# Kernel tuning notes

Measured on AMD Instinct MI355X. Metric: run time of the kernel, lower is better.

## Reference

```python
import math
import jax, jax.numpy as jnp
import numpy as np

B, S, DIM = 1, 2048, 2880
N_HEADS, N_KV, HD = 64, 8, 64
ROPE_FACTOR = 32.0
THETA = 150000.0
NEG_INF = -1e30


def setup_inputs() -> dict:
    key = jax.random.key(0)
    ks = jax.random.split(key, 12)
    std = 0.02
    x = jax.random.normal(ks[0], (B, S, DIM), jnp.float32)
    # rope cache: (S, 2*HD) = [cos | sin], rotate_half convention (angles duplicated)
    inv_freq = 1.0 / (THETA ** (np.arange(0, HD, 2, dtype=np.float32) / HD))
    angles = np.arange(S, dtype=np.float32)[:, None] * inv_freq[None, :]   # (S, HD/2)
    emb = np.concatenate([angles, angles], axis=-1)                        # (S, HD)
    rope_cache = jnp.asarray(np.concatenate([np.cos(emb), np.sin(emb)], axis=-1))  # (S, 2*HD)
    wq_w = jax.random.normal(ks[1], (N_HEADS * HD, DIM), jnp.float32) * std
    wq_b = jax.random.normal(ks[2], (N_HEADS * HD,), jnp.float32) * std
    wk_w = jax.random.normal(ks[3], (N_KV * HD, DIM), jnp.float32) * std
    wk_b = jax.random.normal(ks[4], (N_KV * HD,), jnp.float32) * std
    wv_w = jax.random.normal(ks[5], (N_KV * HD, DIM), jnp.float32) * std
    wv_b = jax.random.normal(ks[6], (N_KV * HD,), jnp.float32) * std
    wo_w = jax.random.normal(ks[7], (DIM, N_HEADS * HD), jnp.float32) * std
    wo_b = jax.random.normal(ks[8], (DIM,), jnp.float32) * std
    sinks = jax.random.normal(ks[9], (N_HEADS,), jnp.float32) * std
    return {"x": x, "rope_cache": rope_cache, "wq_w": wq_w, "wq_b": wq_b,
            "wk_w": wk_w, "wk_b": wk_b, "wv_w": wv_w, "wv_b": wv_b,
            "wo_w": wo_w, "wo_b": wo_b, "sinks": sinks, "sliding_window": 128}


def _rotate_half(t):
    t1, t2 = t[..., : HD // 2], t[..., HD // 2 :]
    return jnp.concatenate([-t2, t1], axis=-1)


def reference(x, rope_cache, wq_w, wq_b, wk_w, wk_b, wv_w, wv_b, wo_w, wo_b, sinks, sliding_window):
    bsz, seqlen, _ = x.shape
    mscale = 0.1 * math.log(ROPE_FACTOR) + 1.0
    scale = mscale / math.sqrt(HD)

    q = (x @ wq_w.T + wq_b).reshape(bsz, seqlen, N_HEADS, HD)
    k = (x @ wk_w.T + wk_b).reshape(bsz, seqlen, N_KV, HD)
    v = (x @ wv_w.T + wv_b).reshape(bsz, seqlen, N_KV, HD)

    cos = rope_cache[:seqlen, :HD][None, :, None, :]   # (1,S,1,HD)
    sin = rope_cache[:seqlen, HD:][None, :, None, :]
    q = q * cos + _rotate_half(q) * sin
    k = k * cos + _rotate_half(k) * sin

    q = q.transpose(0, 2, 1, 3)                        # (B,H,S,hd)
    n_rep = N_HEADS // N_KV
    k = jnp.repeat(k.transpose(0, 2, 1, 3), n_rep, axis=1)  # GQA expand
    v = jnp.repeat(v.transpose(0, 2, 1, 3), n_rep, axis=1)

    scores = jnp.einsum("bhqd,bhkd->bhqk", q, k) * scale
    i = jnp.arange(seqlen)[:, None]
    j = jnp.arange(seqlen)[None, :]
    mask = (j <= i) & ((i - j) < sliding_window)       # causal + sliding window
    scores = jnp.where(mask[None, None], scores, NEG_INF)

    lse = jax.nn.logsumexp(scores, axis=-1)            # (B,H,S)
    attn = jax.nn.softmax(scores, axis=-1)
    out = jnp.einsum("bhqk,bhkd->bhqd", attn, v)

    sink_scale = jax.nn.sigmoid(lse - sinks[None, :, None])[..., None]
    out = out * sink_scale

    out = out.transpose(0, 2, 1, 3).reshape(bsz, seqlen, N_HEADS * HD)
    return out @ wo_w.T + wo_b
```

## Files before the change

### kernel.cpp

```cpp
#include <hip/hip_runtime.h>
#include <hip/hip_bf16.h>
#include <math.h>


typedef __bf16 bf16x8 __attribute__((ext_vector_type(8)));
typedef float  f32x4  __attribute__((ext_vector_type(4)));

#define MFMA_BF16(a,b,c) __builtin_amdgcn_mfma_f32_16x16x32_bf16((a),(b),(c),0,0,0)

__device__ __forceinline__ void gld_lds16(const void* g, void* l) {
    __builtin_amdgcn_global_load_lds(
        (__attribute__((address_space(1))) void*)(g),
        (__attribute__((address_space(3))) void*)(l), 16, 0, 0);
}

__device__ __forceinline__ bf16x8 ld8f(const float* p) {
    f32x4 a = *(const f32x4*)p;
    f32x4 b = *(const f32x4*)(p + 4);
    bf16x8 r;
#pragma unroll
    for (int t = 0; t < 4; t++) { r[t] = (__bf16)a[t]; r[t + 4] = (__bf16)b[t]; }
    return r;
}

__global__ __launch_bounds__(256) void convert_kernel(
    const float* __restrict__ x,  const float* __restrict__ wq,
    const float* __restrict__ wk, const float* __restrict__ wv,
    const float* __restrict__ wo, __bf16* __restrict__ dst)
{
    long e = ((long)blockIdx.x * 256 + threadIdx.x) * 8;
    const float* src; long off;
    if      (e <  5898240L) { src = x;  off = e; }
    else if (e < 17694720L) { src = wq; off = e -  5898240L; }
    else if (e < 19169280L) { src = wk; off = e - 17694720L; }
    else if (e < 20643840L) { src = wv; off = e - 19169280L; }
    else                    { src = wo; off = e - 20643840L; }
    *(bf16x8*)(dst + e) = ld8f(src + off);
}

template <typename TO>
__device__ __forceinline__ void gemm_block64(
    const __bf16* __restrict__ A, const __bf16* __restrict__ W,
    const float* __restrict__ bias, TO* __restrict__ C,
    int N, int Ks, int kBeg, int kEnd, int m0, int n0,
    __bf16* As, __bf16* Bs)
{
    const int tid  = threadIdx.x;
    const int lane = tid & 63;
    const int wv   = tid >> 6;
    const int wm   = (wv >> 1) * 64;
    const int wn   = (wv & 1) * 64;
    const int quad = lane >> 4;
    const int c    = lane & 15;

    const int srow = tid >> 2;
    const int scol = (tid & 3) * 8;

    int br0 = n0 + srow;      if (br0 > N - 1) br0 = N - 1;
    int br1 = n0 + 64 + srow; if (br1 > N - 1) br1 = N - 1;
    const __bf16* pa0 = A + (size_t)(m0 + srow) * Ks + scol;
    const __bf16* pa1 = A + (size_t)(m0 + 64 + srow) * Ks + scol;
    const __bf16* pb0 = W + (size_t)br0 * Ks + scol;
    const __bf16* pb1 = W + (size_t)br1 * Ks + scol;

    f32x4 acc[4][4];
#pragma unroll
    for (int i = 0; i < 4; i++)
#pragma unroll
        for (int j = 0; j < 4; j++) acc[i][j] = (f32x4){0.f, 0.f, 0.f, 0.f};

    for (int kk = kBeg; kk < kEnd; kk += 64) {
        gld_lds16(pa0 + kk,      As + tid * 8);
        gld_lds16(pa1 + kk,      As + 2048 + tid * 8);
        gld_lds16(pa0 + kk + 32, As + 4096 + tid * 8);
        gld_lds16(pa1 + kk + 32, As + 6144 + tid * 8);
        gld_lds16(pb0 + kk,      Bs + tid * 8);
        gld_lds16(pb1 + kk,      Bs + 2048 + tid * 8);
        gld_lds16(pb0 + kk + 32, Bs + 4096 + tid * 8);
        gld_lds16(pb1 + kk + 32, Bs + 6144 + tid * 8);
        __syncthreads();
        for (int kt = 0; kt < 2; kt++) {
            bf16x8 af[4], bfv[4];
#pragma unroll
            for (int i = 0; i < 4; i++)
                af[i] = *(const bf16x8*)&As[kt * 4096 + (wm + i * 16 + c) * 32 + quad * 8];
#pragma unroll
            for (int j = 0; j < 4; j++)
                bfv[j] = *(const bf16x8*)&Bs[kt * 4096 + (wn + j * 16 + c) * 32 + quad * 8];
#pragma unroll
            for (int i = 0; i < 4; i++)
#pragma unroll
                for (int j = 0; j < 4; j++)
                    acc[i][j] = MFMA_BF16(af[i], bfv[j], acc[i][j]);
        }
        __syncthreads();
    }

#pragma unroll
    for (int j = 0; j < 4; j++) {
        int col = n0 + wn + j * 16 + c;
        if (col >= N) continue;
        float bv = bias ? bias[col] : 0.0f;
#pragma unroll
        for (int i = 0; i < 4; i++) {
            int row = m0 + wm + i * 16 + quad * 4;
#pragma unroll
            for (int r = 0; r < 4; r++)
                C[(size_t)(row + r) * N + col] = (TO)(acc[i][j][r] + bv);
        }
    }
}

__global__ __launch_bounds__(256, 3) void qkv_kernel(
    const __bf16* __restrict__ x,
    const __bf16* __restrict__ wq, const float* __restrict__ bq,
    const __bf16* __restrict__ wk, const float* __restrict__ bk,
    const __bf16* __restrict__ wv, const float* __restrict__ bv,
    __bf16* __restrict__ qo, __bf16* __restrict__ ko, __bf16* __restrict__ vo)
{
    __shared__ __align__(16) __bf16 As[8192], Bs[8192];
    const int by = blockIdx.y;
    const __bf16 *W; const float* bias; __bf16* C; int N, n0;
    if (by < 32)      { W = wq; bias = bq; C = qo; N = 4096; n0 = by * 128; }
    else if (by < 36) { W = wk; bias = bk; C = ko; N = 512;  n0 = (by - 32) * 128; }
    else              { W = wv; bias = bv; C = vo; N = 512;  n0 = (by - 36) * 128; }
    gemm_block64<__bf16>(x, W, bias, C, N, 2880, 0, 2880,
                         blockIdx.x * 128, n0, As, Bs);
}

__global__ __launch_bounds__(256, 3) void oproj_kernel(
    const __bf16* __restrict__ a, const __bf16* __restrict__ w,
    __bf16* __restrict__ p0, __bf16* __restrict__ p1)
{
    __shared__ __align__(16) __bf16 As[8192], Bs[8192];
    const int z = blockIdx.z;
    __bf16* C = z ? p1 : p0;
    gemm_block64<__bf16>(a, w, nullptr, C, 2880, 4096, z * 2048, (z + 1) * 2048,
                         blockIdx.x * 128, blockIdx.y * 128, As, Bs);
}

__global__ __launch_bounds__(256) void reduce_kernel(
    const __bf16* __restrict__ p0, const __bf16* __restrict__ p1,
    const float* __restrict__ bo, float* __restrict__ out)
{
    long e = ((long)blockIdx.x * 256 + threadIdx.x) * 8;
    int col = (int)(e % 2880L);
    bf16x8 a = *(const bf16x8*)(p0 + e);
    bf16x8 b = *(const bf16x8*)(p1 + e);
    f32x4 o0, o1;
#pragma unroll
    for (int t = 0; t < 4; t++) {
        o0[t] = (float)a[t]     + (float)b[t]     + bo[col + t];
        o1[t] = (float)a[4 + t] + (float)b[4 + t] + bo[col + 4 + t];
    }
    *(f32x4*)(out + e)     = o0;
    *(f32x4*)(out + e + 4) = o1;
}

__global__ __launch_bounds__(256) void rope_kernel(
    __bf16* __restrict__ qb, __bf16* __restrict__ kb,
    const float* __restrict__ rope)
{
    int idx  = blockIdx.x * 256 + threadIdx.x;
    int dg   = idx & 3;
    int head = (idx >> 2) % 72;
    int s    = (idx >> 2) / 72;
    __bf16* p = (head < 64) ? (qb + (size_t)s * 4096 + head * 64)
                            : (kb + (size_t)s * 512 + (size_t)(head - 64) * 64);
    int d0 = dg * 8;
    bf16x8 x1 = *(bf16x8*)(p + d0);
    bf16x8 x2 = *(bf16x8*)(p + d0 + 32);
    const float* rc = rope + (size_t)s * 128 + d0;
    bf16x8 o1, o2;
#pragma unroll
    for (int t = 0; t < 8; t++) {
        float cc = rc[t], si = rc[64 + t];
        float a = (float)x1[t], b = (float)x2[t];
        o1[t] = (__bf16)(a * cc - b * si);
        o2[t] = (__bf16)(b * cc + a * si);
    }
    *(bf16x8*)(p + d0)      = o1;
    *(bf16x8*)(p + d0 + 32) = o2;
}

__global__ __launch_bounds__(256) void attn_kernel(
    __bf16* __restrict__ q, const __bf16* __restrict__ k,
    const __bf16* __restrict__ v, const float* __restrict__ sinks)
{
    __shared__ __align__(16) char smem[63488];
    __bf16* Qs = (__bf16*)smem;
    __bf16* Ks = (__bf16*)(smem + 9216);
    __bf16* Vt = (__bf16*)(smem + 36864);
    __bf16* P  = (__bf16*)smem;

    const int tid = threadIdx.x, lane = tid & 63, w = tid >> 6;
    const int quad = lane >> 4, c = lane & 15;
    const int i0 = blockIdx.x * 64;
    const int h  = blockIdx.y;
    const int kvh = h >> 3;
    const int k0 = i0 - 128;

    {
        const int row = tid >> 3;
        const int col = (tid & 7) * 8;
#pragma unroll
        for (int it = 0; it < 2; it++) {
            int r2 = row + it * 32;
            bf16x8 t = *(const bf16x8*)(q + (size_t)(i0 + r2) * 4096 + h * 64 + col);
            *(bf16x8*)&Qs[r2 * 72 + col] = t;
        }
#pragma unroll
        for (int it = 0; it < 6; it++) {
            int r2 = row + it * 32;
            int j = k0 + r2; if (j < 0) j = 0;
            bf16x8 t = *(const bf16x8*)(k + (size_t)j * 512 + kvh * 64 + col);
            *(bf16x8*)&Ks[r2 * 72 + col] = t;
        }
        const int vrow = tid & 31;
        const int d0 = (tid >> 5) * 8;
#pragma unroll
        for (int it = 0; it < 6; it++) {
            int r2 = vrow + it * 32;
            int j = k0 + r2; if (j < 0) j = 0;
            bf16x8 t = *(const bf16x8*)(v + (size_t)j * 512 + kvh * 64 + d0);
#pragma unroll
            for (int u = 0; u < 8; u++) Vt[(d0 + u) * 208 + r2] = t[u];
        }
    }
    __syncthreads();

    f32x4 acc[12];
#pragma unroll
    for (int j = 0; j < 12; j++) acc[j] = (f32x4){0.f, 0.f, 0.f, 0.f};
#pragma unroll
    for (int kt = 0; kt < 2; kt++) {
        bf16x8 af = *(const bf16x8*)&Qs[(w * 16 + c) * 72 + kt * 32 + quad * 8];
#pragma unroll
        for (int j = 0; j < 12; j++) {
            bf16x8 bv = *(const bf16x8*)&Ks[(j * 16 + c) * 72 + kt * 32 + quad * 8];
            acc[j] = MFMA_BF16(af, bv, acc[j]);
        }
    }
    __syncthreads();

    const float scale = 0.16832169878499658f;
    const int igb = i0 + w * 16 + quad * 4;
    float rmax[4] = {-3.0e4f, -3.0e4f, -3.0e4f, -3.0e4f};
#pragma unroll
    for (int j = 0; j < 12; j++) {
        int jg = k0 + j * 16 + c;
#pragma unroll
        for (int r = 0; r < 4; r++) {
            int ig = igb + r;
            bool ok = (jg >= 0) && (jg <= ig) && (ig - jg < 128);
            float vv = ok ? acc[j][r] * scale : -3.0e4f;
            acc[j][r] = vv;
            rmax[r] = fmaxf(rmax[r], vv);
        }
    }
#pragma unroll
    for (int off = 1; off < 16; off <<= 1)
#pragma unroll
        for (int r = 0; r < 4; r++)
            rmax[r] = fmaxf(rmax[r], __shfl_xor(rmax[r], off));

    float rs[4] = {0.f, 0.f, 0.f, 0.f};
#pragma unroll
    for (int j = 0; j < 12; j++)
#pragma unroll
        for (int r = 0; r < 4; r++) {
            float e = __expf(acc[j][r] - rmax[r]);
            acc[j][r] = e;
            rs[r] += e;
        }
#pragma unroll
    for (int off = 1; off < 16; off <<= 1)
#pragma unroll
        for (int r = 0; r < 4; r++)
            rs[r] += __shfl_xor(rs[r], off);

    float rowfac[4];
    {
        float sk = sinks[h];
#pragma unroll
        for (int r = 0; r < 4; r++) {
            float s = fmaxf(rs[r], 1e-20f);
            float lse = rmax[r] + __logf(s);
            rowfac[r] = 1.f / ((1.f + __expf(sk - lse)) * s);
        }
    }

#pragma unroll
    for (int j = 0; j < 12; j++)
#pragma unroll
        for (int r = 0; r < 4; r++)
            P[(w * 16 + quad * 4 + r) * 208 + j * 16 + c] = (__bf16)acc[j][r];
    __syncthreads();

    f32x4 acc2[4];
#pragma unroll
    for (int jd = 0; jd < 4; jd++) acc2[jd] = (f32x4){0.f, 0.f, 0.f, 0.f};
#pragma unroll
    for (int kt = 0; kt < 6; kt++) {
        bf16x8 a = *(const bf16x8*)&P[(w * 16 + c) * 208 + kt * 32 + quad * 8];
#pragma unroll
        for (int jd = 0; jd < 4; jd++) {
            bf16x8 b = *(const bf16x8*)&Vt[(jd * 16 + c) * 208 + kt * 32 + quad * 8];
            acc2[jd] = MFMA_BF16(a, b, acc2[jd]);
        }
    }
#pragma unroll
    for (int jd = 0; jd < 4; jd++)
#pragma unroll
        for (int r = 0; r < 4; r++) {
            int qr = w * 16 + quad * 4 + r;
            q[(size_t)(i0 + qr) * 4096 + h * 64 + jd * 16 + c] =
                (__bf16)(acc2[jd][r] * rowfac[r]);
        }
}

extern "C" void kernel_launch(void* const* d_in, const int* in_sizes, int n_in,
                              void* d_out, int out_size, void* d_ws, size_t ws_size,
                              hipStream_t stream) {
    const float* x    = (const float*)d_in[0];
    const float* rope = (const float*)d_in[1];
    const float* wq   = (const float*)d_in[2];
    const float* bq   = (const float*)d_in[3];
    const float* wk   = (const float*)d_in[4];
    const float* bk   = (const float*)d_in[5];
    const float* wv   = (const float*)d_in[6];
    const float* bv   = (const float*)d_in[7];
    const float* wo   = (const float*)d_in[8];
    const float* bo   = (const float*)d_in[9];
    const float* sk   = (const float*)d_in[10];
    float* out = (float*)d_out;

    __bf16* wsb = (__bf16*)d_ws;
    __bf16* xb  = wsb;
    __bf16* wqb = wsb +  5898240L;
    __bf16* wkb = wsb + 17694720L;
    __bf16* wvb = wsb + 19169280L;
    __bf16* wob = wsb + 20643840L;
    __bf16* qb  = wsb + 32440320L;
    __bf16* kb  = wsb + 40828928L;
    __bf16* vb  = wsb + 41877504L;
    __bf16* p0  = wsb;
    __bf16* p1  = wsb +  5898240L;

    convert_kernel<<<15840, 256, 0, stream>>>(x, wq, wk, wv, wo, xb);
    qkv_kernel<<<dim3(16, 40), 256, 0, stream>>>(xb, wqb, bq, wkb, bk, wvb, bv,
                                                 qb, kb, vb);
    rope_kernel<<<2304, 256, 0, stream>>>(qb, kb, rope);
    attn_kernel<<<dim3(32, 64), 256, 0, stream>>>(qb, kb, vb, sk);
    oproj_kernel<<<dim3(16, 23, 2), 256, 0, stream>>>(qb, wob, p0, p1);
    reduce_kernel<<<2880, 256, 0, stream>>>(p0, p1, bo, out);
}
```

Baseline: 349.3 us.

## Split-K the QKV projection with fused reduce+RoPE, and 3-way split o-proj

```diff
diff --git a/kernel.cpp b/kernel.cpp
--- a/kernel.cpp
+++ b/kernel.cpp
@@ -7,6 +7,19 @@
 typedef float  f32x4  __attribute__((ext_vector_type(4)));
 
 #define MFMA_BF16(a,b,c) __builtin_amdgcn_mfma_f32_16x16x32_bf16((a),(b),(c),0,0,0)
+
+#define XB   0L
+#define WQB  5898240L
+#define WKB  17694720L
+#define WVB  19169280L
+#define WOB  20643840L
+#define QB   32440320L
+#define KB   40828928L
+#define VB   41877504L
+#define PQ0  42926080L
+#define PK0  51314688L
+#define PV0  52363264L
+#define SPLIT_BYTES 106823680UL
 
 __device__ __forceinline__ void gld_lds16(const void* g, void* l) {
     __builtin_amdgcn_global_load_lds(
@@ -30,18 +43,17 @@
 {
     long e = ((long)blockIdx.x * 256 + threadIdx.x) * 8;
     const float* src; long off;
-    if      (e <  5898240L) { src = x;  off = e; }
-    else if (e < 17694720L) { src = wq; off = e -  5898240L; }
-    else if (e < 19169280L) { src = wk; off = e - 17694720L; }
-    else if (e < 20643840L) { src = wv; off = e - 19169280L; }
-    else                    { src = wo; off = e - 20643840L; }
+    if      (e <  WQB) { src = x;  off = e; }
+    else if (e <  WKB) { src = wq; off = e - WQB; }
+    else if (e <  WVB) { src = wk; off = e - WKB; }
+    else if (e <  WOB) { src = wv; off = e - WVB; }
+    else               { src = wo; off = e - WOB; }
     *(bf16x8*)(dst + e) = ld8f(src + off);
 }
 
-template <typename TO>
 __device__ __forceinline__ void gemm_block64(
     const __bf16* __restrict__ A, const __bf16* __restrict__ W,
-    const float* __restrict__ bias, TO* __restrict__ C,
+    const float* __restrict__ bias, __bf16* __restrict__ C,
     int N, int Ks, int kBeg, int kEnd, int m0, int n0,
     __bf16* As, __bf16* Bs)
 {
@@ -106,7 +118,7 @@
             int row = m0 + wm + i * 16 + quad * 4;
 #pragma unroll
             for (int r = 0; r < 4; r++)
-                C[(size_t)(row + r) * N + col] = (TO)(acc[i][j][r] + bv);
+                C[(size_t)(row + r) * N + col] = (__bf16)(acc[i][j][r] + bv);
         }
     }
 }
@@ -116,45 +128,106 @@
     const __bf16* __restrict__ wq, const float* __restrict__ bq,
     const __bf16* __restrict__ wk, const float* __restrict__ bk,
     const __bf16* __restrict__ wv, const float* __restrict__ bv,
-    __bf16* __restrict__ qo, __bf16* __restrict__ ko, __bf16* __restrict__ vo)
+    __bf16* __restrict__ qo, __bf16* __restrict__ ko, __bf16* __restrict__ vo,
+    __bf16* __restrict__ pq, __bf16* __restrict__ pk, __bf16* __restrict__ pv,
+    int z0End, int mode)
 {
     __shared__ __align__(16) __bf16 As[8192], Bs[8192];
-    const int by = blockIdx.y;
-    const __bf16 *W; const float* bias; __bf16* C; int N, n0;
-    if (by < 32)      { W = wq; bias = bq; C = qo; N = 4096; n0 = by * 128; }
-    else if (by < 36) { W = wk; bias = bk; C = ko; N = 512;  n0 = (by - 32) * 128; }
-    else              { W = wv; bias = bv; C = vo; N = 512;  n0 = (by - 36) * 128; }
-    gemm_block64<__bf16>(x, W, bias, C, N, 2880, 0, 2880,
-                         blockIdx.x * 128, n0, As, Bs);
+    const int by = blockIdx.y, z = blockIdx.z;
+    const __bf16 *W; const float* bias; __bf16 *Cf, *Cp; int N, n0;
+    if (by < 32)      { W = wq; bias = bq; Cf = qo; Cp = pq; N = 4096; n0 = by * 128; }
+    else if (by < 36) { W = wk; bias = bk; Cf = ko; Cp = pk; N = 512;  n0 = (by - 32) * 128; }
+    else              { W = wv; bias = bv; Cf = vo; Cp = pv; N = 512;  n0 = (by - 36) * 128; }
+    __bf16* C; const float* bu; int kB, kE;
+    if (mode == 0)    { C = Cf; bu = bias;    kB = 0;     kE = 2880; }
+    else if (z == 0)  { C = Cp; bu = nullptr; kB = 0;     kE = z0End; }
+    else              { C = Cf; bu = nullptr; kB = z0End; kE = 2880; }
+    gemm_block64(x, W, bu, C, N, 2880, kB, kE, blockIdx.x * 128, n0, As, Bs);
 }
 
 __global__ __launch_bounds__(256, 3) void oproj_kernel(
     const __bf16* __restrict__ a, const __bf16* __restrict__ w,
-    __bf16* __restrict__ p0, __bf16* __restrict__ p1)
+    __bf16* __restrict__ p0, __bf16* __restrict__ p1, __bf16* __restrict__ p2)
 {
     __shared__ __align__(16) __bf16 As[8192], Bs[8192];
     const int z = blockIdx.z;
-    __bf16* C = z ? p1 : p0;
-    gemm_block64<__bf16>(a, w, nullptr, C, 2880, 4096, z * 2048, (z + 1) * 2048,
-                         blockIdx.x * 128, blockIdx.y * 128, As, Bs);
-}
-
-__global__ __launch_bounds__(256) void reduce_kernel(
+    __bf16* C = (z == 0) ? p0 : (z == 1) ? p1 : p2;
+    const int kB = (z == 0) ? 0 : (z == 1) ? 1408 : 2816;
+    const int kE = (z == 0) ? 1408 : (z == 1) ? 2816 : 4096;
+    gemm_block64(a, w, nullptr, C, 2880, 4096, kB, kE,
+                 blockIdx.x * 128, blockIdx.y * 128, As, Bs);
+}
+
+__global__ __launch_bounds__(256) void reduce3_kernel(
     const __bf16* __restrict__ p0, const __bf16* __restrict__ p1,
-    const float* __restrict__ bo, float* __restrict__ out)
+    const __bf16* __restrict__ p2, const float* __restrict__ bo,
+    float* __restrict__ out)
 {
     long e = ((long)blockIdx.x * 256 + threadIdx.x) * 8;
     int col = (int)(e % 2880L);
     bf16x8 a = *(const bf16x8*)(p0 + e);
     bf16x8 b = *(const bf16x8*)(p1 + e);
+    bf16x8 d = *(const bf16x8*)(p2 + e);
     f32x4 o0, o1;
 #pragma unroll
     for (int t = 0; t < 4; t++) {
-        o0[t] = (float)a[t]     + (float)b[t]     + bo[col + t];
-        o1[t] = (float)a[4 + t] + (float)b[4 + t] + bo[col + 4 + t];
+        o0[t] = (float)a[t] + (float)b[t] + (float)d[t] + bo[col + t];
+        o1[t] = (float)a[4+t] + (float)b[4+t] + (float)d[4+t] + bo[col + 4 + t];
     }
     *(f32x4*)(out + e)     = o0;
     *(f32x4*)(out + e + 4) = o1;
+}
+
+__global__ __launch_bounds__(256) void reduce_rope_kernel(
+    __bf16* __restrict__ qb, __bf16* __restrict__ kb, __bf16* __restrict__ vb,
+    const __bf16* __restrict__ pq, const __bf16* __restrict__ pk,
+    const __bf16* __restrict__ pv,
+    const float* __restrict__ bq, const float* __restrict__ bk,
+    const float* __restrict__ bv, const float* __restrict__ rope)
+{
+    int idx = blockIdx.x * 256 + threadIdx.x;
+    int s   = idx / 320;
+    int r   = idx % 320;
+    if (r < 288) {
+        int head = r >> 2, d0 = (r & 3) * 8;
+        __bf16* f; const __bf16* p; const float* bias;
+        if (head < 64) { f = qb + (size_t)s * 4096 + head * 64;
+                         p = pq + (size_t)s * 4096 + head * 64;
+                         bias = bq + head * 64; }
+        else           { int kh = head - 64;
+                         f = kb + (size_t)s * 512 + kh * 64;
+                         p = pk + (size_t)s * 512 + kh * 64;
+                         bias = bk + kh * 64; }
+        bf16x8 f1 = *(const bf16x8*)(f + d0);
+        bf16x8 f2 = *(const bf16x8*)(f + d0 + 32);
+        bf16x8 p1 = *(const bf16x8*)(p + d0);
+        bf16x8 p2 = *(const bf16x8*)(p + d0 + 32);
+        const float* rc = rope + (size_t)s * 128 + d0;
+        bf16x8 o1, o2;
+#pragma unroll
+        for (int t = 0; t < 8; t++) {
+            float x1 = (float)f1[t] + (float)p1[t] + bias[d0 + t];
+            float x2 = (float)f2[t] + (float)p2[t] + bias[d0 + 32 + t];
+            float cc = rc[t], si = rc[64 + t];
+            o1[t] = (__bf16)(x1 * cc - x2 * si);
+            o2[t] = (__bf16)(x2 * cc + x1 * si);
+        }
+        *(bf16x8*)(f + d0)      = o1;
+        *(bf16x8*)(f + d0 + 32) = o2;
+    } else {
+        int e0 = (r - 288) * 16;
+        size_t e = (size_t)s * 512 + e0;
+#pragma unroll
+        for (int half = 0; half < 2; half++) {
+            bf16x8 a = *(const bf16x8*)(vb + e + half * 8);
+            bf16x8 b = *(const bf16x8*)(pv + e + half * 8);
+            bf16x8 o;
+#pragma unroll
+            for (int t = 0; t < 8; t++)
+                o[t] = (__bf16)((float)a[t] + (float)b[t] + bv[e0 + half * 8 + t]);
+            *(bf16x8*)(vb + e + half * 8) = o;
+        }
+    }
 }
 
 __global__ __launch_bounds__(256) void rope_kernel(
@@ -336,22 +409,35 @@
     float* out = (float*)d_out;
 
     __bf16* wsb = (__bf16*)d_ws;
-    __bf16* xb  = wsb;
-    __bf16* wqb = wsb +  5898240L;
-    __bf16* wkb = wsb + 17694720L;
-    __bf16* wvb = wsb + 19169280L;
-    __bf16* wob = wsb + 20643840L;
-    __bf16* qb  = wsb + 32440320L;
-    __bf16* kb  = wsb + 40828928L;
-    __bf16* vb  = wsb + 41877504L;
-    __bf16* p0  = wsb;
-    __bf16* p1  = wsb +  5898240L;
+    __bf16* xb  = wsb + XB;
+    __bf16* wqb = wsb + WQB;
+    __bf16* wkb = wsb + WKB;
+    __bf16* wvb = wsb + WVB;
+    __bf16* wob = wsb + WOB;
+    __bf16* qb  = wsb + QB;
+    __bf16* kb  = wsb + KB;
+    __bf16* vb  = wsb + VB;
+    __bf16* pq0 = wsb + PQ0;
+    __bf16* pk0 = wsb + PK0;
+    __bf16* pv0 = wsb + PV0;
+    __bf16* po0 = wsb + 0L;
+    __bf16* po1 = wsb + 5898240L;
+    __bf16* po2 = wsb + 11796480L;
+
+    const bool split = (ws_size >= SPLIT_BYTES);
 
     convert_kernel<<<15840, 256, 0, stream>>>(x, wq, wk, wv, wo, xb);
-    qkv_kernel<<<dim3(16, 40), 256, 0, stream>>>(xb, wqb, bq, wkb, bk, wvb, bv,
-                                                 qb, kb, vb);
-    rope_kernel<<<2304, 256, 0, stream>>>(qb, kb, rope);
+    if (split) {
+        qkv_kernel<<<dim3(16, 40, 2), 256, 0, stream>>>(
+            xb, wqb, bq, wkb, bk, wvb, bv, qb, kb, vb, pq0, pk0, pv0, 1472, 1);
+        reduce_rope_kernel<<<2560, 256, 0, stream>>>(
+            qb, kb, vb, pq0, pk0, pv0, bq, bk, bv, rope);
+    } else {
+        qkv_kernel<<<dim3(16, 40, 1), 256, 0, stream>>>(
+            xb, wqb, bq, wkb, bk, wvb, bv, qb, kb, vb, qb, kb, vb, 0, 0);
+        rope_kernel<<<2304, 256, 0, stream>>>(qb, kb, rope);
+    }
     attn_kernel<<<dim3(32, 64), 256, 0, stream>>>(qb, kb, vb, sk);
-    oproj_kernel<<<dim3(16, 23, 2), 256, 0, stream>>>(qb, wob, p0, p1);
-    reduce_kernel<<<2880, 256, 0, stream>>>(p0, p1, bo, out);
-}
+    oproj_kernel<<<dim3(16, 23, 3), 256, 0, stream>>>(qb, wob, po0, po1, po2);
+    reduce3_kernel<<<2880, 256, 0, stream>>>(po0, po1, po2, bo, out);
+}
```

Result: slower. 360.3 us (+3.1%).
